# Kernel optimization log

Measured on AMD Instinct MI355X. Metric: run time of the kernel, lower is better.

## Reference

```python
import jax, jax.numpy as jnp
import numpy as np

NUM_HEADS = 16
EMBED_DIM = 1024
BSZ, T, S = 8, 1024, 1024
NEG_INF = -1e30


def setup_inputs() -> dict:
    key = jax.random.key(0)
    ks = jax.random.split(key, 12)
    E = EMBED_DIM
    decoder_state = jax.random.normal(ks[0], (BSZ, T, E), dtype=jnp.float32)
    source_hids = jax.random.normal(ks[1], (S, BSZ, E), dtype=jnp.float32)
    # realistic padding mask: True = padded position (masked out)
    lengths = jax.random.randint(ks[2], (BSZ,), S // 2, S + 1)
    src_len_mask = jnp.arange(S)[None, :] >= lengths[:, None]  # (BSZ, S) bool
    init = 1.0 / np.sqrt(E)
    Wq = jax.random.uniform(ks[3], (E, E), minval=-init, maxval=init)
    bq = jax.random.uniform(ks[4], (E,), minval=-init, maxval=init)
    Wk = jax.random.uniform(ks[5], (E, E), minval=-init, maxval=init)
    bk = jax.random.uniform(ks[6], (E,), minval=-init, maxval=init)
    Wv = jax.random.uniform(ks[7], (E, E), minval=-init, maxval=init)
    bv = jax.random.uniform(ks[8], (E,), minval=-init, maxval=init)
    Wo = jax.random.uniform(ks[9], (E, E), minval=-init, maxval=init)
    bo = jax.random.uniform(ks[10], (E,), minval=-init, maxval=init)
    return {"decoder_state": decoder_state, "source_hids": source_hids,
            "src_len_mask": src_len_mask, "Wq": Wq, "bq": bq, "Wk": Wk,
            "bk": bk, "Wv": Wv, "bv": bv, "Wo": Wo, "bo": bo}


def reference(decoder_state, source_hids, src_len_mask, Wq, bq, Wk, bk, Wv, bv, Wo, bo):
    B, Tq, E = decoder_state.shape
    Sk = source_hids.shape[0]
    H = NUM_HEADS
    hd = E // H
    scaling = hd ** (-0.5)

    query = jnp.swapaxes(decoder_state, 0, 1)  # (T, B, E)
    q = (query @ Wq.T + bq) * scaling          # (T, B, E)
    k = source_hids @ Wk.T + bk                # (S, B, E)
    v = source_hids @ Wv.T + bv                # (S, B, E)

    q = q.reshape(Tq, B, H, hd)
    k = k.reshape(Sk, B, H, hd)
    v = v.reshape(Sk, B, H, hd)

    scores = jnp.einsum("tbhd,sbhd->bhts", q, k)  # (B, H, T, S)
    scores = jnp.where(src_len_mask[:, None, None, :], NEG_INF, scores)
    weights = jax.nn.softmax(scores, axis=-1)     # (B, H, T, S); dropout p=0

    attn = jnp.einsum("bhts,sbhd->tbhd", weights, v).reshape(Tq, B, E)
    attn = attn @ Wo.T + bo                       # (T, B, E)

    # need_weights: mean over heads -> (B, T, S); then transpose(0,2) -> (S, T, B)
    attn_weights_out = jnp.swapaxes(weights.mean(axis=1), 0, 2)
    # squeeze=True is a no-op here since T != 1
    return attn, attn_weights_out
```

## Files before the change

kernel.cpp:

```cpp
#include <hip/hip_runtime.h>
#include <stdint.h>
#include <stddef.h>

typedef __attribute__((ext_vector_type(8))) short bf16x8;
typedef __attribute__((ext_vector_type(4))) float f32x4;
typedef __attribute__((ext_vector_type(4))) uint32_t u32x4;

#define DEVINL static __device__ __forceinline__

DEVINL float b2f(uint16_t u) {
  uint32_t x = ((uint32_t)u) << 16;
  float f;
  __builtin_memcpy(&f, &x, 4);
  return f;
}

DEVINL uint16_t f2b(float f) {
  uint32_t u;
  __builtin_memcpy(&u, &f, 4);
  return (uint16_t)((u + 0x7fffu + ((u >> 16) & 1u)) >> 16);
}

DEVINL void gload16(const void* gsrc, void* ldst) {
  __builtin_amdgcn_global_load_lds(
      (const __attribute__((address_space(1))) void*)gsrc,
      (__attribute__((address_space(3))) void*)ldst, 16, 0, 0);
}

__global__ void detect_kernel(const void* __restrict__ wq, const void* __restrict__ mask,
                              const void* __restrict__ bq, const void* __restrict__ bk,
                              const void* __restrict__ bv, const void* __restrict__ bo,
                              int* __restrict__ hdr, float* __restrict__ bias) {
  __shared__ int sflag, smask32, slen[8];
  const int tid = threadIdx.x;
  if (tid == 0) { sflag = 0; smask32 = 0; }
  if (tid < 8) slen[tid] = 0;
  __syncthreads();
  const uint16_t* w16 = (const uint16_t*)wq;
  int f = 0;
  for (int i = tid; i < 4096; i += 256) {
    uint16_t u = w16[i];
    uint32_t e = (u >> 7) & 0xFFu;
    if (fabsf(b2f(u)) > 0.25f || e == 0xFFu) f = 1;
  }
  if (f) atomicOr(&sflag, 1);
  const uint8_t* mb = (const uint8_t*)mask;
  int m32 = 0;
  for (int i = tid; i < 8191; i += 256) {
    if ((i & 1023) != 1023 && mb[i] != 0 && mb[i + 1] == 0) m32 = 1;
  }
  if (m32) atomicOr(&smask32, 1);
  __syncthreads();
  if (smask32) {
    const int* mi = (const int*)mask;
    for (int i = tid; i < 8192; i += 256) { if (mi[i] == 0) atomicAdd(&slen[i >> 10], 1); }
  } else {
    for (int i = tid; i < 8192; i += 256) { if (mb[i] == 0) atomicAdd(&slen[i >> 10], 1); }
  }
  __syncthreads();
  if (tid == 0) hdr[0] = sflag;
  if (tid < 8) hdr[1 + tid] = slen[tid];
  const void* bs[4] = {bq, bk, bv, bo};
  for (int j = 0; j < 4; ++j) {
    for (int i = tid; i < 1024; i += 256) {
      float v = sflag ? ((const float*)bs[j])[i] : b2f(((const uint16_t*)bs[j])[i]);
      bias[j * 1024 + i] = v;
    }
  }
}

__global__ __launch_bounds__(256)
void convert_kernel(const void* __restrict__ s0, const void* __restrict__ s1,
                    const void* __restrict__ s2, const void* __restrict__ s3,
                    const void* __restrict__ s4, const void* __restrict__ s5,
                    uint16_t* __restrict__ d0, uint16_t* __restrict__ d1,
                    uint16_t* __restrict__ d2, const int* __restrict__ hdr, int doW) {
  const int isf = hdr[0];
  const size_t n01 = 1048576;
  const size_t nw = 131072;
  const size_t total = doW ? (2 * n01 + 4 * nw) : (2 * n01);
  size_t gid = (size_t)blockIdx.x * 256 + threadIdx.x;
  const size_t stride = (size_t)gridDim.x * 256;
  for (; gid < total; gid += stride) {
    const void* sp;
    uint16_t* dp;
    size_t off;
    if (gid < n01) { sp = s0; dp = d0; off = gid; }
    else if (gid < 2 * n01) { sp = s1; dp = d1; off = gid - n01; }
    else {
      const size_t w = (gid - 2 * n01) >> 17;
      off = (gid - 2 * n01) & (nw - 1);
      sp = (w == 0) ? s2 : (w == 1) ? s3 : (w == 2) ? s4 : s5;
      dp = d2 + w * 1048576;
    }
    if (isf) {
      const float* fp = (const float*)sp + off * 8;
      const f32x4 a = *(const f32x4*)fp;
      const f32x4 c = *(const f32x4*)(fp + 4);
      u32x4 r;
      r[0] = (uint32_t)f2b(a[0]) | ((uint32_t)f2b(a[1]) << 16);
      r[1] = (uint32_t)f2b(a[2]) | ((uint32_t)f2b(a[3]) << 16);
      r[2] = (uint32_t)f2b(c[0]) | ((uint32_t)f2b(c[1]) << 16);
      r[3] = (uint32_t)f2b(c[2]) | ((uint32_t)f2b(c[3]) << 16);
      *(u32x4*)(dp + off * 8) = r;
    } else {
      *(u32x4*)(dp + off * 8) = *(const u32x4*)((const uint16_t*)sp + off * 8);
    }
  }
}

enum { MQ = 0, MK = 1, MV = 2, MO = 3 };

DEVINL u32x4 load8w(const void* __restrict__ src, bool f32, size_t eoff) {
  if (!f32) {
    return *(const u32x4*)((const uint16_t*)src + eoff);
  }
  const float* p = (const float*)src + eoff;
  const f32x4 a = *(const f32x4*)p;
  const f32x4 c = *(const f32x4*)(p + 4);
  u32x4 r;
  r[0] = (uint32_t)f2b(a[0]) | ((uint32_t)f2b(a[1]) << 16);
  r[1] = (uint32_t)f2b(a[2]) | ((uint32_t)f2b(a[3]) << 16);
  r[2] = (uint32_t)f2b(c[0]) | ((uint32_t)f2b(c[1]) << 16);
  r[3] = (uint32_t)f2b(c[2]) | ((uint32_t)f2b(c[3]) << 16);
  return r;
}

template <int MODE>
__global__ __launch_bounds__(256)
void gemm_bt(const uint16_t* __restrict__ Ab, const void* __restrict__ Wr,
             const float* __restrict__ bias, const int* __restrict__ hdr,
             void* __restrict__ outp, float scale, int wIsBf16) {
  constexpr int KD = 1024;
  __shared__ __align__(16) uint16_t lA[128][80];
  __shared__ __align__(16) uint16_t lB[128][80];
  const int tid = threadIdx.x;
  const int bm = blockIdx.x, bn = blockIdx.y;
  const int isf = hdr[0];
  const bool wF32 = (wIsBf16 == 0) && (isf != 0);
  const int lane = tid & 63, wave = tid >> 6;
  const int wm = wave >> 1, wn = wave & 1;
  const int g = lane >> 4, cc = lane & 15;
  const int srow = tid >> 3;
  const int scol = (tid & 7) * 8;

  f32x4 acc[4][4];
#pragma unroll
  for (int i = 0; i < 4; ++i)
#pragma unroll
    for (int j = 0; j < 4; ++j) acc[i][j] = (f32x4){0.f, 0.f, 0.f, 0.f};

  u32x4 ra[4], rb[4];
#pragma unroll
  for (int c = 0; c < 4; ++c) {
    ra[c] = *(const u32x4*)(Ab + (size_t)(bm * 128 + srow + c * 32) * KD + scol);
    rb[c] = load8w(Wr, wF32, (size_t)(bn * 128 + srow + c * 32) * KD + scol);
  }
  for (int kt = 0; kt < KD / 64; ++kt) {
    __syncthreads();
#pragma unroll
    for (int c = 0; c < 4; ++c) {
      *(u32x4*)&lA[srow + c * 32][scol] = ra[c];
      *(u32x4*)&lB[srow + c * 32][scol] = rb[c];
    }
    __syncthreads();
    if (kt + 1 < KD / 64) {
#pragma unroll
      for (int c = 0; c < 4; ++c) {
        ra[c] = *(const u32x4*)(Ab + (size_t)(bm * 128 + srow + c * 32) * KD + (kt + 1) * 64 + scol);
        rb[c] = load8w(Wr, wF32, (size_t)(bn * 128 + srow + c * 32) * KD + (kt + 1) * 64 + scol);
      }
    }
#pragma unroll
    for (int kk = 0; kk < 2; ++kk) {
      bf16x8 af[4], bfr[4];
#pragma unroll
      for (int mi = 0; mi < 4; ++mi) af[mi] = *(const bf16x8*)&lA[wm * 64 + mi * 16 + cc][kk * 32 + g * 8];
#pragma unroll
      for (int ni = 0; ni < 4; ++ni) bfr[ni] = *(const bf16x8*)&lB[wn * 64 + ni * 16 + cc][kk * 32 + g * 8];
#pragma unroll
      for (int mi = 0; mi < 4; ++mi)
#pragma unroll
        for (int ni = 0; ni < 4; ++ni)
          acc[mi][ni] = __builtin_amdgcn_mfma_f32_16x16x32_bf16(af[mi], bfr[ni], acc[mi][ni], 0, 0, 0);
    }
  }
#pragma unroll
  for (int mi = 0; mi < 4; ++mi) {
#pragma unroll
    for (int ni = 0; ni < 4; ++ni) {
      const int col = bn * 128 + wn * 64 + ni * 16 + cc;
      const float bv = bias[col];
      const int r0 = bm * 128 + wm * 64 + mi * 16 + g * 4;
#pragma unroll
      for (int r = 0; r < 4; ++r) {
        const int row = r0 + r;
        const float v = (acc[mi][ni][r] + bv) * scale;
        if (MODE == MQ) {
          const int b = row >> 10, t = row & 1023, h = col >> 6, d = col & 63;
          ((uint16_t*)outp)[(((size_t)(b * 16 + h) << 10) + t) * 64 + d] = f2b(v);
        } else if (MODE == MK) {
          const int s = row >> 3, b = row & 7, h = col >> 6, d = col & 63;
          ((uint16_t*)outp)[(((size_t)(b * 16 + h) << 10) + s) * 64 + d] = f2b(v);
        } else if (MODE == MV) {
          const int s = row >> 3, b = row & 7, h = col >> 6, d = col & 63;
          ((uint16_t*)outp)[(((size_t)(b * 16 + h) << 6) + d) * 1024 + s] = f2b(v);
        } else {
          const size_t o = (size_t)row * 1024 + col;
          if (isf) ((float*)outp)[o] = v;
          else ((uint16_t*)outp)[o] = f2b(v);
        }
      }
    }
  }
}

__global__ __launch_bounds__(1024)
void attn_kernel(const uint16_t* __restrict__ Qh, const uint16_t* __restrict__ Kh,
                 const uint16_t* __restrict__ Vh, const int* __restrict__ hdr,
                 uint16_t* __restrict__ AP, uint16_t* __restrict__ Wm) {
  __shared__ __align__(16) uint16_t kbuf[2][8192];
  __shared__ __align__(16) uint16_t vbuf[2][8192];
  __shared__ __align__(16) uint16_t pstash[32][1024];
  __shared__ float pvx[2][32][68];

  const int tid = threadIdx.x, lane = tid & 63, w = tid >> 6;
  const int g = lane >> 4, cc = lane & 15;
  const int wt = w >> 3, ws = w & 7;
  const int dq = (w >> 1) & 3, ks = w & 1;
  const int b = blockIdx.x & 7, tt = blockIdx.x >> 3;
  const int t0 = tt * 32;
  const int len = hdr[1 + b];
  const int tme = tid >> 5, s5 = tid & 31;

  auto stage = [&](int p, int buf) {
    const int hh = p >> 3, st = p & 7;
    const uint16_t* Kb = Kh + ((size_t)(b * 16 + hh) << 16);
    const uint16_t* Vt = Vh + ((size_t)(b * 16 + hh) << 16);
    {
      const int row = tid >> 3;
      const int c = (tid & 7) ^ (row & 7);
      gload16(Kb + (st * 128 + row) * 64 + c * 8, &kbuf[buf][w * 512]);
    }
    {
      const int d = tid >> 4;
      const int c = tid & 15;
      const int cg = (c & 8) | ((c ^ (d & 7)) & 7);
      gload16(Vt + d * 1024 + st * 128 + cg * 8, &vbuf[buf][w * 512]);
    }
  };

  stage(0, 0);
  asm volatile("s_waitcnt vmcnt(0)" ::: "memory");
  __builtin_amdgcn_sched_barrier(0);
  __builtin_amdgcn_s_barrier();

  float wmean[32];
#pragma unroll
  for (int j = 0; j < 32; ++j) wmean[j] = 0.f;

  for (int h = 0; h < 16; ++h) {
    const uint16_t* Qb = Qh + ((size_t)(b * 16 + h) << 16) + (((size_t)(t0 + wt * 16 + cc)) << 6);
    f32x4 pv = (f32x4){0.f, 0.f, 0.f, 0.f};
    for (int st = 0; st < 8; ++st) {
      const int p = h * 8 + st;
      const int cur = p & 1;
      if (p + 1 < 128) stage(p + 1, cur ^ 1);
      {
        const bf16x8 qf0 = *(const bf16x8*)(Qb + g * 8);
        const bf16x8 qf1 = *(const bf16x8*)(Qb + 32 + g * 8);
        const int row = ws * 16 + cc;
        f32x4 a = (f32x4){0.f, 0.f, 0.f, 0.f};
#pragma unroll
        for (int kk = 0; kk < 2; ++kk) {
          const bf16x8 kf = *(const bf16x8*)&kbuf[cur][row * 64 + (((kk * 4 + g) ^ (cc & 7)) << 3)];
          a = __builtin_amdgcn_mfma_f32_16x16x32_bf16(kk ? qf1 : qf0, kf, a, 0, 0, 0);
        }
        const int s = st * 128 + row;
        const bool msk = (s >= len);
        const int cbase = st * 16 + ws * 2 + (cc >> 3);
#pragma unroll
        for (int r = 0; r < 4; ++r) {
          const float v = msk ? 0.f : __expf(a[r]);
          const int tl = wt * 16 + g * 4 + r;
          const int cs = (cbase & ~7) | ((cbase ^ tl) & 7);
          pstash[tl][(cs << 3) + (cc & 7)] = f2b(v);
        }
      }
      asm volatile("s_waitcnt lgkmcnt(0)" ::: "memory");
      __builtin_amdgcn_sched_barrier(0);
      __builtin_amdgcn_s_barrier();
      {
        const int tr = wt * 16 + cc;
#pragma unroll
        for (int kk = 0; kk < 2; ++kk) {
          const int ca = st * 16 + ks * 8 + kk * 4 + g;
          const int ca2 = (ca & ~7) | ((ca ^ tr) & 7);
          const bf16x8 af = *(const bf16x8*)&pstash[tr][ca2 << 3];
          const int cv = ks * 8 + kk * 4 + g;
          const int cv2 = (cv & 8) | ((cv ^ (cc & 7)) & 7);
          const bf16x8 vf = *(const bf16x8*)&vbuf[cur][(dq * 16 + cc) * 128 + (cv2 << 3)];
          pv = __builtin_amdgcn_mfma_f32_16x16x32_bf16(af, vf, pv, 0, 0, 0);
        }
      }
      __syncthreads();
    }
#pragma unroll
    for (int r = 0; r < 4; ++r)
      pvx[ks][wt * 16 + g * 4 + r][dq * 16 + cc] = pv[r];
    float winv;
    {
      uint32_t p4[16];
#pragma unroll
      for (int q = 0; q < 4; ++q) {
        const int c = s5 * 4 + q;
        const int c2 = (c & ~7) | ((c ^ tme) & 7);
        *(u32x4*)&p4[q * 4] = *(const u32x4*)&pstash[tme][c2 << 3];
      }
      float sm = 0.f;
#pragma unroll
      for (int j = 0; j < 16; ++j) {
        sm += b2f((uint16_t)(p4[j] & 0xffffu));
        sm += b2f((uint16_t)(p4[j] >> 16));
      }
#pragma unroll
      for (int m = 16; m >= 1; m >>= 1) sm += __shfl_xor(sm, m, 64);
      winv = 1.f / sm;
#pragma unroll
      for (int j = 0; j < 16; ++j) {
        wmean[2 * j] += b2f((uint16_t)(p4[j] & 0xffffu)) * winv;
        wmean[2 * j + 1] += b2f((uint16_t)(p4[j] >> 16)) * winv;
      }
    }
    asm volatile("s_waitcnt lgkmcnt(0)" ::: "memory");
    __builtin_amdgcn_sched_barrier(0);
    __builtin_amdgcn_s_barrier();
    {
      const int d0 = s5 * 2;
      const float v0 = (pvx[0][tme][d0] + pvx[1][tme][d0]) * winv;
      const float v1 = (pvx[0][tme][d0 + 1] + pvx[1][tme][d0 + 1]) * winv;
      const uint32_t pk = (uint32_t)f2b(v0) | ((uint32_t)f2b(v1) << 16);
      *(uint32_t*)(AP + ((((size_t)(t0 + tme)) * 8 + b) << 10) + h * 64 + d0) = pk;
    }
  }

  {
    uint16_t ob[32];
#pragma unroll
    for (int j = 0; j < 32; ++j) ob[j] = f2b(wmean[j] * 0.0625f);
    uint16_t* dst = Wm + (((size_t)(b * 1024 + t0 + tme)) << 10) + s5 * 32;
#pragma unroll
    for (int q = 0; q < 4; ++q) *(u32x4*)(dst + q * 8) = *(const u32x4*)&ob[q * 8];
  }
}

__global__ __launch_bounds__(256)
void wtrans_kernel(const uint16_t* __restrict__ Wm, const int* __restrict__ hdr,
                   void* __restrict__ outBase) {
  __shared__ uint16_t lt[8][32][68];
  const int tid = threadIdx.x;
  const int s0 = blockIdx.x * 64, t0 = blockIdx.y * 32;
  const int isf = hdr[0];
  const int rr = tid >> 4;
  const int sc = (tid & 15) * 4;
#pragma unroll
  for (int p = 0; p < 16; ++p) {
    const int row = p * 16 + rr;
    const int b = row >> 5, t = row & 31;
    const uint64_t v = *(const uint64_t*)(Wm + (((size_t)(b * 1024 + t0 + t)) << 10) + s0 + sc);
    *(uint64_t*)&lt[b][t][sc] = v;
  }
  __syncthreads();
#pragma unroll
  for (int p = 0; p < 8; ++p) {
    const int pair = p * 256 + tid;
    const int t = pair & 31, s = pair >> 5;
    const size_t o = 8388608 + ((size_t)(s0 + s) * 1024 + (t0 + t)) * 8;
    if (isf) {
      f32x4 v0, v1;
#pragma unroll
      for (int b = 0; b < 4; ++b) v0[b] = b2f(lt[b][t][s]);
#pragma unroll
      for (int b = 0; b < 4; ++b) v1[b] = b2f(lt[b + 4][t][s]);
      *(f32x4*)((float*)outBase + o) = v0;
      *(f32x4*)((float*)outBase + o + 4) = v1;
    } else {
      u32x4 v;
#pragma unroll
      for (int q = 0; q < 4; ++q)
        v[q] = (uint32_t)lt[2 * q][t][s] | ((uint32_t)lt[2 * q + 1][t][s] << 16);
      *(u32x4*)((uint16_t*)outBase + o) = v;
    }
  }
}

__global__ void fill_pattern(uint32_t* p, size_t n) {
  size_t i = (size_t)blockIdx.x * 256 + threadIdx.x;
  const size_t stride = (size_t)gridDim.x * 256;
  for (; i < n; i += stride) p[i] = 0x3f3f3f3fu;
}

extern "C" void kernel_launch(void* const* d_in, const int* in_sizes, int n_in,
                              void* d_out, int out_size, void* d_ws, size_t ws_size,
                              hipStream_t stream) {
  char* ws = (char*)d_ws;
  int* hdr = (int*)ws;
  float* bias = (float*)(ws + 4096);
  uint16_t* Q = (uint16_t*)(ws + (1u << 20));
  uint16_t* K = Q + 8388608;
  uint16_t* V = K + 8388608;
  uint16_t* AP = V + 8388608;
  uint16_t* Wm = AP + 8388608;
  uint16_t* dec_b = AP;
  uint16_t* src_b = Wm;
  const size_t needBase = (1ull << 20) + 5ull * 16777216ull;
  const size_t needFull = needBase + 8ull * 1048576ull;
  uint16_t* Wb = (uint16_t*)(ws + needBase);
  const int useConvW = (ws_size >= needFull) ? 1 : 0;
  if (ws_size < needBase) {
    fill_pattern<<<1024, 256, 0, stream>>>((uint32_t*)d_out, (size_t)out_size / 2);
    return;
  }

  detect_kernel<<<1, 256, 0, stream>>>(d_in[3], d_in[2], d_in[4], d_in[6], d_in[8], d_in[10], hdr, bias);

  convert_kernel<<<4096, 256, 0, stream>>>(d_in[0], d_in[1], d_in[3], d_in[5], d_in[7], d_in[9],
                                           dec_b, src_b, Wb, hdr, useConvW);

  const void* Wq = useConvW ? (const void*)(Wb + 0 * 1048576) : (const void*)d_in[3];
  const void* Wk = useConvW ? (const void*)(Wb + 1 * 1048576) : (const void*)d_in[5];
  const void* Wv = useConvW ? (const void*)(Wb + 2 * 1048576) : (const void*)d_in[7];
  const void* Wo = useConvW ? (const void*)(Wb + 3 * 1048576) : (const void*)d_in[9];

  dim3 gg(64, 8);
  gemm_bt<MQ><<<gg, 256, 0, stream>>>(dec_b, Wq, bias, hdr, Q, 0.125f, useConvW);
  gemm_bt<MK><<<gg, 256, 0, stream>>>(src_b, Wk, bias + 1024, hdr, K, 1.f, useConvW);
  gemm_bt<MV><<<gg, 256, 0, stream>>>(src_b, Wv, bias + 2048, hdr, V, 1.f, useConvW);

  attn_kernel<<<256, 1024, 0, stream>>>(Q, K, V, hdr, AP, Wm);

  wtrans_kernel<<<dim3(16, 32), 256, 0, stream>>>(Wm, hdr, d_out);

  gemm_bt<MO><<<gg, 256, 0, stream>>>(AP, Wo, bias + 3072, hdr, d_out, 1.f, useConvW);
}
```

Measured before the change: 348.7 us.

## Use direct global-to-LDS loads in GEMM and rework attention loop barriers

The GEMM now loads A (and bf16 W) tiles straight into XOR-swizzled LDS with global_load_lds instead of staging through registers, which drops the register prefetch and therefore the overlap of the next tile's load with compute. In the attention kernel, the Q fragment loads are hoisted out of the inner loop, and the per-step trailing __syncthreads is replaced by a vmcnt wait plus barrier at the top of each step. The pstash row-sum read and the Wm mean store are reindexed to interleaved 16-byte chunks, so consecutive lanes write contiguous memory. The GEMM change also serialises the load and compute phases within each k-step.

Result: faster. 303.4 us (-13.0%).

```diff
diff --git a/kernel.cpp b/kernel.cpp
--- a/kernel.cpp
+++ b/kernel.cpp
@@ -131,18 +131,16 @@
 void gemm_bt(const uint16_t* __restrict__ Ab, const void* __restrict__ Wr,
              const float* __restrict__ bias, const int* __restrict__ hdr,
              void* __restrict__ outp, float scale, int wIsBf16) {
-  constexpr int KD = 1024;
-  __shared__ __align__(16) uint16_t lA[128][80];
-  __shared__ __align__(16) uint16_t lB[128][80];
-  const int tid = threadIdx.x;
+  __shared__ __align__(16) uint16_t lA[8192];
+  __shared__ __align__(16) uint16_t lB[8192];
+  const int tid = threadIdx.x, lane = tid & 63, wave = tid >> 6;
   const int bm = blockIdx.x, bn = blockIdx.y;
   const int isf = hdr[0];
   const bool wF32 = (wIsBf16 == 0) && (isf != 0);
-  const int lane = tid & 63, wave = tid >> 6;
   const int wm = wave >> 1, wn = wave & 1;
   const int g = lane >> 4, cc = lane & 15;
-  const int srow = tid >> 3;
-  const int scol = (tid & 7) * 8;
+  const int lr = lane >> 3, lc = lane & 7;
+  const int scc = (lc ^ lr) * 8;
 
   f32x4 acc[4][4];
 #pragma unroll
@@ -150,34 +148,41 @@
 #pragma unroll
     for (int j = 0; j < 4; ++j) acc[i][j] = (f32x4){0.f, 0.f, 0.f, 0.f};
 
-  u32x4 ra[4], rb[4];
-#pragma unroll
-  for (int c = 0; c < 4; ++c) {
-    ra[c] = *(const u32x4*)(Ab + (size_t)(bm * 128 + srow + c * 32) * KD + scol);
-    rb[c] = load8w(Wr, wF32, (size_t)(bn * 128 + srow + c * 32) * KD + scol);
-  }
-  for (int kt = 0; kt < KD / 64; ++kt) {
+  for (int kt = 0; kt < 16; ++kt) {
     __syncthreads();
 #pragma unroll
-    for (int c = 0; c < 4; ++c) {
-      *(u32x4*)&lA[srow + c * 32][scol] = ra[c];
-      *(u32x4*)&lB[srow + c * 32][scol] = rb[c];
+    for (int q = 0; q < 4; ++q) {
+      const int j = wave * 4 + q;
+      gload16(Ab + (size_t)(bm * 128 + j * 8 + lr) * 1024 + kt * 64 + scc, &lA[j * 512]);
+    }
+    if (!wF32) {
+#pragma unroll
+      for (int q = 0; q < 4; ++q) {
+        const int j = wave * 4 + q;
+        gload16((const uint16_t*)Wr + (size_t)(bn * 128 + j * 8 + lr) * 1024 + kt * 64 + scc, &lB[j * 512]);
+      }
+    } else {
+#pragma unroll
+      for (int q = 0; q < 4; ++q) {
+        const int j = wave * 4 + q;
+        const u32x4 rv = load8w(Wr, true, (size_t)(bn * 128 + j * 8 + lr) * 1024 + kt * 64 + lc * 8);
+        *(u32x4*)&lB[j * 512 + lr * 64 + ((lc ^ lr) * 8)] = rv;
+      }
     }
     __syncthreads();
-    if (kt + 1 < KD / 64) {
-#pragma unroll
-      for (int c = 0; c < 4; ++c) {
-        ra[c] = *(const u32x4*)(Ab + (size_t)(bm * 128 + srow + c * 32) * KD + (kt + 1) * 64 + scol);
-        rb[c] = load8w(Wr, wF32, (size_t)(bn * 128 + srow + c * 32) * KD + (kt + 1) * 64 + scol);
-      }
-    }
 #pragma unroll
     for (int kk = 0; kk < 2; ++kk) {
       bf16x8 af[4], bfr[4];
 #pragma unroll
-      for (int mi = 0; mi < 4; ++mi) af[mi] = *(const bf16x8*)&lA[wm * 64 + mi * 16 + cc][kk * 32 + g * 8];
-#pragma unroll
-      for (int ni = 0; ni < 4; ++ni) bfr[ni] = *(const bf16x8*)&lB[wn * 64 + ni * 16 + cc][kk * 32 + g * 8];
+      for (int mi = 0; mi < 4; ++mi) {
+        const int row = wm * 64 + mi * 16 + cc;
+        af[mi] = *(const bf16x8*)&lA[row * 64 + (((kk * 4 + g) ^ (cc & 7)) << 3)];
+      }
+#pragma unroll
+      for (int ni = 0; ni < 4; ++ni) {
+        const int row = wn * 64 + ni * 16 + cc;
+        bfr[ni] = *(const bf16x8*)&lB[row * 64 + (((kk * 4 + g) ^ (cc & 7)) << 3)];
+      }
 #pragma unroll
       for (int mi = 0; mi < 4; ++mi)
 #pragma unroll
@@ -251,9 +256,6 @@
   };
 
   stage(0, 0);
-  asm volatile("s_waitcnt vmcnt(0)" ::: "memory");
-  __builtin_amdgcn_sched_barrier(0);
-  __builtin_amdgcn_s_barrier();
 
   float wmean[32];
 #pragma unroll
@@ -261,14 +263,17 @@
 
   for (int h = 0; h < 16; ++h) {
     const uint16_t* Qb = Qh + ((size_t)(b * 16 + h) << 16) + (((size_t)(t0 + wt * 16 + cc)) << 6);
+    const bf16x8 qf0 = *(const bf16x8*)(Qb + g * 8);
+    const bf16x8 qf1 = *(const bf16x8*)(Qb + 32 + g * 8);
     f32x4 pv = (f32x4){0.f, 0.f, 0.f, 0.f};
     for (int st = 0; st < 8; ++st) {
       const int p = h * 8 + st;
       const int cur = p & 1;
+      asm volatile("s_waitcnt vmcnt(0)" ::: "memory");
+      __builtin_amdgcn_sched_barrier(0);
+      __builtin_amdgcn_s_barrier();
       if (p + 1 < 128) stage(p + 1, cur ^ 1);
       {
-        const bf16x8 qf0 = *(const bf16x8*)(Qb + g * 8);
-        const bf16x8 qf1 = *(const bf16x8*)(Qb + 32 + g * 8);
         const int row = ws * 16 + cc;
         f32x4 a = (f32x4){0.f, 0.f, 0.f, 0.f};
 #pragma unroll
@@ -303,7 +308,6 @@
           pv = __builtin_amdgcn_mfma_f32_16x16x32_bf16(af, vf, pv, 0, 0, 0);
         }
       }
-      __syncthreads();
     }
 #pragma unroll
     for (int r = 0; r < 4; ++r)
@@ -313,7 +317,7 @@
       uint32_t p4[16];
 #pragma unroll
       for (int q = 0; q < 4; ++q) {
-        const int c = s5 * 4 + q;
+        const int c = s5 + 32 * q;
         const int c2 = (c & ~7) | ((c ^ tme) & 7);
         *(u32x4*)&p4[q * 4] = *(const u32x4*)&pstash[tme][c2 << 3];
       }
@@ -345,12 +349,14 @@
   }
 
   {
-    uint16_t ob[32];
-#pragma unroll
-    for (int j = 0; j < 32; ++j) ob[j] = f2b(wmean[j] * 0.0625f);
-    uint16_t* dst = Wm + (((size_t)(b * 1024 + t0 + tme)) << 10) + s5 * 32;
-#pragma unroll
-    for (int q = 0; q < 4; ++q) *(u32x4*)(dst + q * 8) = *(const u32x4*)&ob[q * 8];
+    uint16_t* dst = Wm + (((size_t)(b * 1024 + t0 + tme)) << 10);
+#pragma unroll
+    for (int q = 0; q < 4; ++q) {
+      uint16_t ob[8];
+#pragma unroll
+      for (int e = 0; e < 8; ++e) ob[e] = f2b(wmean[q * 8 + e] * 0.0625f);
+      *(u32x4*)(dst + q * 256 + s5 * 8) = *(const u32x4*)ob;
+    }
   }
 }
 
```
